# Performance work log

Hardware: AMD Instinct MI355X
Metric: run time of the kernel (lower is better)

## Reference

```python
import jax, jax.numpy as jnp
import numpy as np

B, T, C = 4, 4096, 512


def setup_inputs() -> dict:
    key = jax.random.key(0)
    ks = jax.random.split(key, 7)
    s = 1.0 / np.sqrt(C)  # ~ torch Linear init scale
    X = jax.random.normal(ks[0], (B, T, C), jnp.float32)
    S_n = jnp.zeros((B, C, C), jnp.float32)
    W_Q = jax.random.normal(ks[1], (C, C), jnp.float32) * s
    b_Q = jax.random.normal(ks[2], (C,), jnp.float32) * s
    W_K = jax.random.normal(ks[3], (C, C), jnp.float32) * s
    b_K = jax.random.normal(ks[4], (C,), jnp.float32) * s
    W_V = jax.random.normal(ks[5], (C, C), jnp.float32) * s
    b_V = jax.random.normal(ks[6], (C,), jnp.float32) * s
    return {"X": X, "S_n": S_n, "W_Q": W_Q, "b_Q": b_Q,
            "W_K": W_K, "b_K": b_K, "W_V": W_V, "b_V": b_V}


def reference(X, S_n, W_Q, b_Q, W_K, b_K, W_V, b_V):
    # forward_chunkwise with chunk_len = 1 (exact simplification):
    #   per step t (gamma g_t from linspace(0.96, 0.99, T)):
    #     inner_t = (q_t . k_t) * v_t            # D = gamma^0 = 1
    #     cross_t = (q_t @ S) * g_t              # e[:,0,:] = g^1
    #     O_t     = tanh(inner_t + cross_t)
    #     S      <- k_t^T v_t + g_t * S          # D[-1] = 1, g**chunk_len = g
    Bx, Tx, Cx = X.shape
    Q = X @ W_Q + b_Q  # [B,T,C]
    K = X @ W_K + b_K
    V = X @ W_V + b_V
    gammas = jnp.linspace(0.96, 0.99, Tx).astype(X.dtype)

    def step(S, inp):
        q, k, v, g = inp  # q,k,v: [B,C]; g: scalar
        inner = jnp.sum(q * k, axis=-1, keepdims=True) * v      # [B,C]
        cross = jnp.einsum('bc,bcd->bd', q, S) * g              # [B,C]
        O = jnp.tanh(inner + cross)
        S_new = jnp.einsum('bc,bd->bcd', k, v) + S * g          # [B,C,C]
        return S_new, O

    # original resets S_n to zeros regardless of the passed-in value
    S0 = jnp.zeros_like(S_n)
    S_final, O = jax.lax.scan(
        step, S0,
        (Q.transpose(1, 0, 2), K.transpose(1, 0, 2), V.transpose(1, 0, 2), gammas))
    out = O.transpose(1, 0, 2)  # [B,T,C]
    return out, S_final
```

## Files before the change

### kernel.cpp

```cpp
#include <hip/hip_runtime.h>
#include <math.h>

#define Bsz  4
#define Tlen 4096
#define Cdim 512
#define CUT  (-12.0f)
#define NBE  8388608

typedef unsigned int u32;
typedef _Float16 f16;
typedef __attribute__((ext_vector_type(8))) _Float16 f16x8;
typedef __attribute__((ext_vector_type(4))) float floatx4;
#define MFMA_F16(a,b,c) __builtin_amdgcn_mfma_f32_16x16x32_f16((a),(b),(c),0,0,0)

union pun8 { uint4 u; f16x8 f; };

__device__ __forceinline__ u32 pack2(f16 a, f16 b) {
    return (u32)__builtin_bit_cast(unsigned short, a) |
           ((u32)__builtin_bit_cast(unsigned short, b) << 16);
}
__device__ __forceinline__ u32 splitpack(float v) {
    f16 h = (f16)v;
    f16 l = (f16)(v - (float)h);
    return pack2(h, l);
}
__device__ __forceinline__ void unpack8(const u32* p, f16x8& h, f16x8& l) {
    uint4 q0 = *(const uint4*)p;
    uint4 q1 = *(const uint4*)(p + 4);
    pun8 ph, pl;
    ph.u.x = __builtin_amdgcn_perm(q0.y, q0.x, 0x05040100u);
    pl.u.x = __builtin_amdgcn_perm(q0.y, q0.x, 0x07060302u);
    ph.u.y = __builtin_amdgcn_perm(q0.w, q0.z, 0x05040100u);
    pl.u.y = __builtin_amdgcn_perm(q0.w, q0.z, 0x07060302u);
    ph.u.z = __builtin_amdgcn_perm(q1.y, q1.x, 0x05040100u);
    pl.u.z = __builtin_amdgcn_perm(q1.y, q1.x, 0x07060302u);
    ph.u.w = __builtin_amdgcn_perm(q1.w, q1.z, 0x05040100u);
    pl.u.w = __builtin_amdgcn_perm(q1.w, q1.z, 0x07060302u);
    h = ph.f; l = pl.f;
}
__device__ __forceinline__ float tanh_fast(float x) {
    return 1.0f - 2.0f / (__expf(2.0f * x) + 1.0f);
}

__global__ __launch_bounds__(256) void prep_kernel(
    const float* __restrict__ X,
    const float* __restrict__ WQ, const float* __restrict__ WK,
    const float* __restrict__ WV,
    f16* __restrict__ Xf, f16* __restrict__ WT,
    float* __restrict__ Lg, float* __restrict__ Wfin, int* __restrict__ sLo) {
    __shared__ char pshm[18432];
    int bid = blockIdx.x, tid = threadIdx.x;
    if (bid < 2048) {
        size_t i = ((size_t)bid * 256 + tid) * 16;
        float v[16];
#pragma unroll
        for (int j = 0; j < 4; ++j) {
            float4 a = *(const float4*)(X + i + j * 4);
            v[j*4+0]=a.x; v[j*4+1]=a.y; v[j*4+2]=a.z; v[j*4+3]=a.w;
        }
        uint4 o0, o1;
        o0.x = pack2((f16)v[0], (f16)v[1]);   o0.y = pack2((f16)v[2], (f16)v[3]);
        o0.z = pack2((f16)v[4], (f16)v[5]);   o0.w = pack2((f16)v[6], (f16)v[7]);
        o1.x = pack2((f16)v[8], (f16)v[9]);   o1.y = pack2((f16)v[10], (f16)v[11]);
        o1.z = pack2((f16)v[12], (f16)v[13]); o1.w = pack2((f16)v[14], (f16)v[15]);
        *(uint4*)(Xf + i) = o0;
        *(uint4*)(Xf + i + 8) = o1;
    } else if (bid < 2240) {
        f16* tile = (f16*)pshm;
        int wb = bid - 2048;
        int mat = wb >> 6, rem = wb & 63;
        int k0 = (rem >> 3) * 64, n0 = (rem & 7) * 64;
        const float* W = (mat == 0) ? WQ : (mat == 1) ? WK : WV;
        int row = tid >> 2, q = tid & 3;
        const float* src = W + (size_t)(k0 + row) * Cdim + n0 + q * 16;
        float vv[16];
#pragma unroll
        for (int j = 0; j < 4; ++j) {
            float4 v = *(const float4*)(src + j * 4);
            vv[j*4+0]=v.x; vv[j*4+1]=v.y; vv[j*4+2]=v.z; vv[j*4+3]=v.w;
        }
#pragma unroll
        for (int j = 0; j < 16; ++j) tile[(q * 16 + j) * 72 + row] = (f16)vv[j];
        __syncthreads();
        f16x8 r0 = *(const f16x8*)(tile + row * 72 + q * 16);
        f16x8 r1 = *(const f16x8*)(tile + row * 72 + q * 16 + 8);
        f16* dst = WT + ((size_t)mat * Cdim + n0 + row) * Cdim + k0 + q * 16;
        *(f16x8*)dst = r0;
        *(f16x8*)(dst + 8) = r1;
    } else {
        float* Lsh = (float*)pshm;
        float* sums = (float*)(pshm + 16400);
        float lg[16];
        float local = 0.f;
        int base = tid * 16;
#pragma unroll
        for (int i = 0; i < 16; ++i) {
            int t = base + i;
            float g = 0.96f + 0.03f * ((float)t * (1.0f / 4095.0f));
            lg[i] = logf(g);
            local += lg[i];
        }
        sums[tid] = local;
        __syncthreads();
        for (int off = 1; off < 256; off <<= 1) {
            float v = sums[tid];
            if (tid >= off) v += sums[tid - off];
            __syncthreads();
            sums[tid] = v;
            __syncthreads();
        }
        float pre = (tid == 0) ? 0.f : sums[tid - 1];
#pragma unroll
        for (int i = 0; i < 16; ++i) {
            Lsh[base + i] = pre;
            pre += lg[i];
        }
        if (tid == 255) Lsh[4096] = pre;
        __syncthreads();
        for (int t = tid; t < 4097; t += 256) Lg[t] = Lsh[t];
        float LT = Lsh[4096];
        for (int s = tid; s < 4096; s += 256) Wfin[s] = __expf(LT - Lsh[s + 1]);
        if (tid < 128) {
            float ref = Lsh[tid * 32 + 1];
            int st_hi = tid >> 2;
            int lo = st_hi;
            for (int st = 0; st < st_hi; ++st)
                if (ref - Lsh[st * 128 + 128] > CUT) { lo = st; break; }
            sLo[tid] = lo;
        }
    }
}

__global__ __launch_bounds__(256, 2) void qkv_mfma(
    const f16* __restrict__ Xf, const f16* __restrict__ WT,
    const float* __restrict__ bQ, const float* __restrict__ bK,
    const float* __restrict__ bV,
    f16* __restrict__ Qf, f16* __restrict__ Kf,
    f16* __restrict__ KT, f16* __restrict__ VT) {
    __shared__ char smem[34816];
    u32* sX = (u32*)smem;
    u32* sW = (u32*)(smem + 16384);
    f16* sB = (f16*)smem;
    f16* T  = (f16*)smem;

    int tid = threadIdx.x, lane = tid & 63, wid = tid >> 6;
    int l16 = lane & 15, quad = lane >> 4;
    int wm = wid & 1, wn = wid >> 1;
    int xb = blockIdx.x;
    int mat = xb >> 2, n0 = (xb & 3) * 128;
    int m0 = blockIdx.y * 128;

    floatx4 acc[4][4];
#pragma unroll
    for (int i = 0; i < 4; ++i)
#pragma unroll
        for (int j = 0; j < 4; ++j) acc[i][j] = (floatx4)0.f;

    int srow = tid >> 1, shalf = tid & 1;
    int arow_a = wm * 64 + l16, arow_b = wn * 64 + l16;
    int swz_f = (l16 & 7) << 2;

    for (int kc = 0; kc < Cdim; kc += 64) {
        __syncthreads();
        {
            const f16* gx = Xf + (size_t)(m0 + srow) * Cdim + kc + shalf * 32;
            const f16* gw = WT + ((size_t)(mat * Cdim) + n0 + srow) * Cdim + kc + shalf * 32;
            int wswz = (srow & 7) << 2;
#pragma unroll
            for (int k = 0; k < 4; ++k) {
                uint4 xv = *(const uint4*)(gx + k * 8);
                uint4 wv = *(const uint4*)(gw + k * 8);
                int w = shalf * 16 + k * 4;
                *(uint4*)&sX[srow * 32 + (w ^ wswz)] = xv;
                *(uint4*)&sW[srow * 32 + (w ^ wswz)] = wv;
            }
        }
        __syncthreads();
#pragma unroll
        for (int ks = 0; ks < 2; ++ks) {
            int w0 = ks * 16 + quad * 4;
            f16x8 af[4], bf[4];
#pragma unroll
            for (int mt = 0; mt < 4; ++mt)
                af[mt] = ((pun8*)&sX[(arow_a + mt * 16) * 32 + (w0 ^ swz_f)])->f;
#pragma unroll
            for (int nt = 0; nt < 4; ++nt)
                bf[nt] = ((pun8*)&sW[(arow_b + nt * 16) * 32 + (w0 ^ swz_f)])->f;
#pragma unroll
            for (int mt = 0; mt < 4; ++mt)
#pragma unroll
                for (int nt = 0; nt < 4; ++nt)
                    acc[mt][nt] = MFMA_F16(af[mt], bf[nt], acc[mt][nt]);
        }
    }

    const float* bias = (mat == 0) ? bQ : (mat == 1) ? bK : bV;
    float bv[4];
#pragma unroll
    for (int nt = 0; nt < 4; ++nt) bv[nt] = bias[n0 + wn * 64 + nt * 16 + l16];
    float cv[4][4][4];
#pragma unroll
    for (int mt = 0; mt < 4; ++mt)
#pragma unroll
        for (int nt = 0; nt < 4; ++nt)
#pragma unroll
            for (int r = 0; r < 4; ++r) cv[mt][nt][r] = acc[mt][nt][r] + bv[nt];

    int b = m0 >> 12, tloc = m0 & 4095;

    if (mat == 2) {
        __syncthreads();
#pragma unroll
        for (int mt = 0; mt < 4; ++mt)
#pragma unroll
            for (int nt = 0; nt < 4; ++nt) {
                int dl = wn * 64 + nt * 16 + l16;
                int tl = wm * 64 + mt * 16 + quad * 4;
                *(u32*)(T + dl * 134 + tl)     = pack2((f16)cv[mt][nt][0], (f16)cv[mt][nt][1]);
                *(u32*)(T + dl * 134 + tl + 2) = pack2((f16)cv[mt][nt][2], (f16)cv[mt][nt][3]);
            }
        __syncthreads();
#pragma unroll 8
        for (int dd = 0; dd < 32; ++dd) {
            int dl = wid * 32 + dd;
            u32 v = *(const u32*)(T + dl * 134 + lane * 2);
            *(u32*)(VT + ((size_t)(b * Cdim + n0 + dl)) * Tlen + tloc + lane * 2) = v;
        }
    } else {
        __syncthreads();
#pragma unroll
        for (int mt = 0; mt < 4; ++mt)
#pragma unroll
            for (int nt = 0; nt < 4; ++nt)
#pragma unroll
                for (int r = 0; r < 4; ++r)
                    sB[(wm * 64 + mt * 16 + quad * 4 + r) * 136 +
                       wn * 64 + nt * 16 + l16] = (f16)cv[mt][nt][r];
        __syncthreads();
        {
            f16* Out = (mat == 0) ? Qf : Kf;
            int r2 = tid >> 1, h2 = tid & 1;
            f16* dst = Out + (size_t)(m0 + r2) * Cdim + n0 + h2 * 64;
#pragma unroll
            for (int j = 0; j < 8; ++j)
                *(uint4*)(dst + j * 8) = *(const uint4*)(sB + r2 * 136 + h2 * 64 + j * 8);
        }
        if (mat == 1) {
            __syncthreads();
#pragma unroll
            for (int mt = 0; mt < 4; ++mt)
#pragma unroll
                for (int nt = 0; nt < 4; ++nt) {
                    int dl = wn * 64 + nt * 16 + l16;
                    int tl = wm * 64 + mt * 16 + quad * 4;
                    *(u32*)(T + dl * 134 + tl)     = pack2((f16)cv[mt][nt][0], (f16)cv[mt][nt][1]);
                    *(u32*)(T + dl * 134 + tl + 2) = pack2((f16)cv[mt][nt][2], (f16)cv[mt][nt][3]);
                }
            __syncthreads();
#pragma unroll 8
            for (int dd = 0; dd < 32; ++dd) {
                int dl = wid * 32 + dd;
                u32 v = *(const u32*)(T + dl * 134 + lane * 2);
                *(u32*)(KT + ((size_t)(b * Cdim + n0 + dl)) * Tlen + tloc + lane * 2) = v;
            }
        }
    }
}

__global__ __launch_bounds__(512, 4) void attn_mfma(
    const f16* __restrict__ Qf, const f16* __restrict__ Kf,
    const f16* __restrict__ VT, const float* __restrict__ Lg,
    const int* __restrict__ sLo, float* __restrict__ out) {
    __shared__ char smem[49664];
    u32* sQ  = (u32*)smem;
    u32* sPc = (u32*)(smem + 32768);

    int tid = threadIdx.x, lane = tid & 63, wid = tid >> 6;
    int l16 = lane & 15, quad = lane >> 4;

    int i = blockIdx.x;
    int halfsel = i >> 8, q = i & 255;
    int L = ((q & 7) << 5) | (q >> 3);
    int b = L >> 6, ttl = L & 63;
    int tt = halfsel ? (63 - ttl) : (64 + ttl);
    int t0 = tt * 32;
    size_t bT = (size_t)b * Tlen;
    int lo = sLo[tt], hi = tt >> 2;

    {
        int r = tid >> 4, c16 = tid & 15;
        const f16* src = Qf + (bT + t0 + r) * Cdim + c16 * 32;
        int wswz = (r & 7) << 2;
#pragma unroll
        for (int k = 0; k < 4; ++k) {
            uint4 v = *(const uint4*)(src + k * 8);
            int w = c16 * 16 + k * 4;
            *(uint4*)&sQ[r * 256 + (w ^ wswz)] = v;
        }
    }

    float aT[2][4];
#pragma unroll
    for (int mt = 0; mt < 2; ++mt)
#pragma unroll
        for (int r = 0; r < 4; ++r)
            aT[mt][r] = Lg[t0 + mt * 16 + quad * 4 + r + 1];

    floatx4 oacc[2][4];
#pragma unroll
    for (int mt = 0; mt < 2; ++mt)
#pragma unroll
        for (int nt = 0; nt < 4; ++nt) oacc[mt][nt] = (floatx4)0.f;

    int swz_f = (l16 & 7) << 2;
    int rowA0 = l16 * 256;
    int rowA1 = (16 + l16) * 256;

    __syncthreads();

    for (int st = lo; st <= hi; ++st) {
        int s0 = st * 128;
        float lsp = Lg[s0 + wid * 16 + l16 + 1];

        floatx4 pacc[2];
        pacc[0] = (floatx4)0.f; pacc[1] = (floatx4)0.f;

        const f16* kb = Kf + (bT + s0 + wid * 16 + l16) * Cdim;
#pragma unroll 4
        for (int kc = 0; kc < 16; ++kc) {
            int ko = kc * 32 + quad * 8;
            int w0 = kc * 16 + quad * 4;
            f16x8 a0 = ((pun8*)&sQ[rowA0 + (w0 ^ swz_f)])->f;
            f16x8 a1 = ((pun8*)&sQ[rowA1 + (w0 ^ swz_f)])->f;
            f16x8 bk = *(const f16x8*)(kb + ko);
            pacc[0] = MFMA_F16(a0, bk, pacc[0]);
            pacc[1] = MFMA_F16(a1, bk, pacc[1]);
        }

        __syncthreads();
#pragma unroll
        for (int mt = 0; mt < 2; ++mt)
#pragma unroll
            for (int r = 0; r < 4; ++r) {
                int tl = mt * 16 + quad * 4 + r;
                int sl = wid * 16 + l16;
                int t = t0 + tl, s = s0 + sl;
                float p = pacc[mt][r];
                p = (s <= t) ? p * __expf(aT[mt][r] - lsp) : 0.f;
                sPc[tl * 132 + (sl ^ ((tl & 7) << 4))] = splitpack(p);
            }
        __syncthreads();

        const f16* vb = VT + ((size_t)(b * Cdim + wid * 64 + l16)) * Tlen + s0;
#pragma unroll
        for (int kf = 0; kf < 4; ++kf) {
            int sb = kf * 32 + quad * 8;
            f16x8 ph[2], pl[2];
#pragma unroll
            for (int mt = 0; mt < 2; ++mt) {
                int tl = mt * 16 + l16;
                unpack8(&sPc[tl * 132 + (sb ^ ((tl & 7) << 4))], ph[mt], pl[mt]);
            }
#pragma unroll
            for (int nt = 0; nt < 4; ++nt) {
                f16x8 vf = *(const f16x8*)(vb + (size_t)nt * 16 * Tlen + sb);
#pragma unroll
                for (int mt = 0; mt < 2; ++mt) {
                    oacc[mt][nt] = MFMA_F16(ph[mt], vf, oacc[mt][nt]);
                    oacc[mt][nt] = MFMA_F16(pl[mt], vf, oacc[mt][nt]);
                }
            }
        }
    }

#pragma unroll
    for (int mt = 0; mt < 2; ++mt)
#pragma unroll
        for (int nt = 0; nt < 4; ++nt)
#pragma unroll
            for (int r = 0; r < 4; ++r) {
                int t = t0 + mt * 16 + quad * 4 + r;
                int d = wid * 64 + nt * 16 + l16;
                out[(bT + t) * (size_t)Cdim + d] = tanh_fast(oacc[mt][nt][r]);
            }
}

__global__ __launch_bounds__(256) void sfinal_mfma(
    const f16* __restrict__ KT, const f16* __restrict__ VT,
    const float* __restrict__ Lg, const float* __restrict__ Wfin,
    float* __restrict__ S) {
    __shared__ f16 sA[64 * 72];
    __shared__ f16 sB2[128 * 72];
    int tid = threadIdx.x, lane = tid & 63, wid = tid >> 6;
    int l16 = lane & 15, quad = lane >> 4;
    int wv_c = wid >> 1, wv_d = wid & 1;
    int c0 = blockIdx.x * 64, d0 = blockIdx.y * 128, bb = blockIdx.z;
    float LT = Lg[Tlen];
    floatx4 acc[2][4];
#pragma unroll
    for (int i = 0; i < 2; ++i)
#pragma unroll
        for (int jj = 0; jj < 4; ++jj) acc[i][jj] = (floatx4)0.f;

    int s0start = Tlen - 64;
    for (int s0 = 0; s0 < Tlen; s0 += 64)
        if (LT - Lg[s0 + 64] > CUT) { s0start = s0; break; }

    int rowA = tid >> 2, qA = (tid & 3) * 16;
    int rowB = tid >> 1, qB = (tid & 1) * 32;
    for (int s0 = s0start; s0 < Tlen; s0 += 64) {
        __syncthreads();
        {
            const f16* g = KT + ((size_t)(bb * Cdim + c0 + rowA)) * Tlen + s0 + qA;
            f16x8 u0 = *(const f16x8*)g;
            f16x8 u1 = *(const f16x8*)(g + 8);
            float wv[16];
#pragma unroll
            for (int jj = 0; jj < 4; ++jj) {
                float4 w4 = *(const float4*)(Wfin + s0 + qA + jj * 4);
                wv[jj*4+0]=w4.x; wv[jj*4+1]=w4.y; wv[jj*4+2]=w4.z; wv[jj*4+3]=w4.w;
            }
            f16x8 o0, o1;
#pragma unroll
            for (int jj = 0; jj < 8; ++jj) o0[jj] = (f16)((float)u0[jj] * wv[jj]);
#pragma unroll
            for (int jj = 0; jj < 8; ++jj) o1[jj] = (f16)((float)u1[jj] * wv[8 + jj]);
            *(f16x8*)(sA + rowA * 72 + qA) = o0;
            *(f16x8*)(sA + rowA * 72 + qA + 8) = o1;
            const f16* gv = VT + ((size_t)(bb * Cdim + d0 + rowB)) * Tlen + s0 + qB;
#pragma unroll
            for (int jj = 0; jj < 4; ++jj)
                *(uint4*)(sB2 + rowB * 72 + qB + jj * 8) = *(const uint4*)(gv + jj * 8);
        }
        __syncthreads();
#pragma unroll
        for (int ks = 0; ks < 2; ++ks) {
            int ko = ks * 32 + quad * 8;
            f16x8 av[2], bv2[4];
#pragma unroll
            for (int ct = 0; ct < 2; ++ct)
                av[ct] = *(const f16x8*)(sA + (wv_c * 32 + ct * 16 + l16) * 72 + ko);
#pragma unroll
            for (int dt = 0; dt < 4; ++dt)
                bv2[dt] = *(const f16x8*)(sB2 + (wv_d * 64 + dt * 16 + l16) * 72 + ko);
#pragma unroll
            for (int ct = 0; ct < 2; ++ct)
#pragma unroll
                for (int dt = 0; dt < 4; ++dt)
                    acc[ct][dt] = MFMA_F16(av[ct], bv2[dt], acc[ct][dt]);
        }
    }
#pragma unroll
    for (int ct = 0; ct < 2; ++ct)
#pragma unroll
        for (int dt = 0; dt < 4; ++dt)
#pragma unroll
            for (int r = 0; r < 4; ++r) {
                int c = c0 + wv_c * 32 + ct * 16 + quad * 4 + r;
                int d = d0 + wv_d * 64 + dt * 16 + l16;
                S[((size_t)(bb * Cdim + c)) * Cdim + d] = acc[ct][dt][r];
            }
}

extern "C" void kernel_launch(void* const* d_in, const int* in_sizes, int n_in,
                              void* d_out, int out_size, void* d_ws, size_t ws_size,
                              hipStream_t stream) {
    (void)in_sizes; (void)n_in; (void)out_size; (void)ws_size;
    const float* X  = (const float*)d_in[0];
    const float* WQ = (const float*)d_in[2];
    const float* bQ = (const float*)d_in[3];
    const float* WK = (const float*)d_in[4];
    const float* bK = (const float*)d_in[5];
    const float* WV = (const float*)d_in[6];
    const float* bV = (const float*)d_in[7];

    float* out   = (float*)d_out;
    float* S_out = out + (size_t)NBE;

    char* ws = (char*)d_ws;
    f16*   Xf   = (f16*)(ws);
    f16*   Qf   = (f16*)(ws + 2ull * NBE);
    f16*   Kf   = (f16*)(ws + 4ull * NBE);
    f16*   KT   = (f16*)(ws + 6ull * NBE);
    f16*   VT   = (f16*)(ws + 8ull * NBE);
    f16*   WT   = (f16*)(ws + 10ull * NBE);
    char*  tail = ws + 10ull * NBE + (2u << 20);
    float* Lg   = (float*)(tail);
    float* Wfin = (float*)(tail + 16512);
    int*   sLo  = (int*)(tail + 16512 + 16384);

    prep_kernel<<<2241, 256, 0, stream>>>(X, WQ, WK, WV, Xf, WT, Lg, Wfin, sLo);
    qkv_mfma<<<dim3(12, 128), 256, 0, stream>>>(Xf, WT, bQ, bK, bV, Qf, Kf, KT, VT);
    attn_mfma<<<512, 512, 0, stream>>>(Qf, Kf, VT, Lg, sLo, out);
    sfinal_mfma<<<dim3(8, 4, Bsz), 256, 0, stream>>>(KT, VT, Lg, Wfin, S_out);
}
```

Baseline: 264.8 us.

## Halve attention query tile to 16 rows and double block count

The chunked attention kernel now processes 16 query rows per block instead of 32. It launches 1024 blocks with half the shared memory and a higher occupancy bound, and the per-tile band start indices are recomputed for 256 tiles. The aim is better load balance across CUs for the causal, band-limited workload and more resident waves. In exchange, each K and V fragment loaded from global memory is reused across half as many query rows, which raises total K/V traffic.

```diff
diff --git a/kernel.cpp b/kernel.cpp
--- a/kernel.cpp
+++ b/kernel.cpp
@@ -120,9 +120,9 @@
         for (int t = tid; t < 4097; t += 256) Lg[t] = Lsh[t];
         float LT = Lsh[4096];
         for (int s = tid; s < 4096; s += 256) Wfin[s] = __expf(LT - Lsh[s + 1]);
-        if (tid < 128) {
-            float ref = Lsh[tid * 32 + 1];
-            int st_hi = tid >> 2;
+        {
+            float ref = Lsh[tid * 16 + 1];
+            int st_hi = tid >> 3;
             int lo = st_hi;
             for (int st = 0; st < st_hi; ++st)
                 if (ref - Lsh[st * 128 + 128] > CUT) { lo = st; break; }
@@ -267,54 +267,49 @@
     }
 }
 
-__global__ __launch_bounds__(512, 4) void attn_mfma(
+__global__ __launch_bounds__(512, 8) void attn_mfma(
     const f16* __restrict__ Qf, const f16* __restrict__ Kf,
     const f16* __restrict__ VT, const float* __restrict__ Lg,
     const int* __restrict__ sLo, float* __restrict__ out) {
-    __shared__ char smem[49664];
-    u32* sQ  = (u32*)smem;
-    u32* sPc = (u32*)(smem + 32768);
+    __shared__ char smem[24832];
+    u32* sQ = (u32*)smem;
+    u32* sP = (u32*)(smem + 16384);
 
     int tid = threadIdx.x, lane = tid & 63, wid = tid >> 6;
     int l16 = lane & 15, quad = lane >> 4;
 
     int i = blockIdx.x;
-    int halfsel = i >> 8, q = i & 255;
-    int L = ((q & 7) << 5) | (q >> 3);
-    int b = L >> 6, ttl = L & 63;
-    int tt = halfsel ? (63 - ttl) : (64 + ttl);
-    int t0 = tt * 32;
+    int halfsel = i >> 9, q = i & 511;
+    int L = ((q & 7) << 6) | (q >> 3);
+    int b = L >> 7, ttl = L & 127;
+    int tt = halfsel ? (127 - ttl) : (128 + ttl);
+    int t0 = tt * 16;
     size_t bT = (size_t)b * Tlen;
-    int lo = sLo[tt], hi = tt >> 2;
+    int lo = sLo[tt], hi = tt >> 3;
 
     {
-        int r = tid >> 4, c16 = tid & 15;
-        const f16* src = Qf + (bT + t0 + r) * Cdim + c16 * 32;
+        int r = tid >> 5, c = tid & 31;
+        const f16* src = Qf + (bT + t0 + r) * Cdim + c * 16;
         int wswz = (r & 7) << 2;
 #pragma unroll
-        for (int k = 0; k < 4; ++k) {
+        for (int k = 0; k < 2; ++k) {
             uint4 v = *(const uint4*)(src + k * 8);
-            int w = c16 * 16 + k * 4;
+            int w = c * 8 + k * 4;
             *(uint4*)&sQ[r * 256 + (w ^ wswz)] = v;
         }
     }
 
-    float aT[2][4];
-#pragma unroll
-    for (int mt = 0; mt < 2; ++mt)
-#pragma unroll
-        for (int r = 0; r < 4; ++r)
-            aT[mt][r] = Lg[t0 + mt * 16 + quad * 4 + r + 1];
-
-    floatx4 oacc[2][4];
-#pragma unroll
-    for (int mt = 0; mt < 2; ++mt)
-#pragma unroll
-        for (int nt = 0; nt < 4; ++nt) oacc[mt][nt] = (floatx4)0.f;
+    float aT[4];
+#pragma unroll
+    for (int r = 0; r < 4; ++r)
+        aT[r] = Lg[t0 + quad * 4 + r + 1];
+
+    floatx4 oacc[4];
+#pragma unroll
+    for (int nt = 0; nt < 4; ++nt) oacc[nt] = (floatx4)0.f;
 
     int swz_f = (l16 & 7) << 2;
     int rowA0 = l16 * 256;
-    int rowA1 = (16 + l16) * 256;
 
     __syncthreads();
 
@@ -322,8 +317,7 @@
         int s0 = st * 128;
         float lsp = Lg[s0 + wid * 16 + l16 + 1];
 
-        floatx4 pacc[2];
-        pacc[0] = (floatx4)0.f; pacc[1] = (floatx4)0.f;
+        floatx4 pacc = (floatx4)0.f;
 
         const f16* kb = Kf + (bT + s0 + wid * 16 + l16) * Cdim;
 #pragma unroll 4
@@ -331,58 +325,45 @@
             int ko = kc * 32 + quad * 8;
             int w0 = kc * 16 + quad * 4;
             f16x8 a0 = ((pun8*)&sQ[rowA0 + (w0 ^ swz_f)])->f;
-            f16x8 a1 = ((pun8*)&sQ[rowA1 + (w0 ^ swz_f)])->f;
             f16x8 bk = *(const f16x8*)(kb + ko);
-            pacc[0] = MFMA_F16(a0, bk, pacc[0]);
-            pacc[1] = MFMA_F16(a1, bk, pacc[1]);
-        }
-
-        __syncthreads();
-#pragma unroll
-        for (int mt = 0; mt < 2; ++mt)
-#pragma unroll
-            for (int r = 0; r < 4; ++r) {
-                int tl = mt * 16 + quad * 4 + r;
-                int sl = wid * 16 + l16;
-                int t = t0 + tl, s = s0 + sl;
-                float p = pacc[mt][r];
-                p = (s <= t) ? p * __expf(aT[mt][r] - lsp) : 0.f;
-                sPc[tl * 132 + (sl ^ ((tl & 7) << 4))] = splitpack(p);
-            }
+            pacc = MFMA_F16(a0, bk, pacc);
+        }
+
+        __syncthreads();
+#pragma unroll
+        for (int r = 0; r < 4; ++r) {
+            int tl = quad * 4 + r;
+            int sl = wid * 16 + l16;
+            int t = t0 + tl, s = s0 + sl;
+            float p = pacc[r];
+            p = (s <= t) ? p * __expf(aT[r] - lsp) : 0.f;
+            sP[tl * 132 + (sl ^ ((tl & 7) << 4))] = splitpack(p);
+        }
         __syncthreads();
 
         const f16* vb = VT + ((size_t)(b * Cdim + wid * 64 + l16)) * Tlen + s0;
 #pragma unroll
         for (int kf = 0; kf < 4; ++kf) {
             int sb = kf * 32 + quad * 8;
-            f16x8 ph[2], pl[2];
-#pragma unroll
-            for (int mt = 0; mt < 2; ++mt) {
-                int tl = mt * 16 + l16;
-                unpack8(&sPc[tl * 132 + (sb ^ ((tl & 7) << 4))], ph[mt], pl[mt]);
-            }
+            f16x8 ph, pl;
+            unpack8(&sP[l16 * 132 + (sb ^ ((l16 & 7) << 4))], ph, pl);
 #pragma unroll
             for (int nt = 0; nt < 4; ++nt) {
                 f16x8 vf = *(const f16x8*)(vb + (size_t)nt * 16 * Tlen + sb);
-#pragma unroll
-                for (int mt = 0; mt < 2; ++mt) {
-                    oacc[mt][nt] = MFMA_F16(ph[mt], vf, oacc[mt][nt]);
-                    oacc[mt][nt] = MFMA_F16(pl[mt], vf, oacc[mt][nt]);
-                }
-            }
-        }
-    }
-
-#pragma unroll
-    for (int mt = 0; mt < 2; ++mt)
-#pragma unroll
-        for (int nt = 0; nt < 4; ++nt)
-#pragma unroll
-            for (int r = 0; r < 4; ++r) {
-                int t = t0 + mt * 16 + quad * 4 + r;
-                int d = wid * 64 + nt * 16 + l16;
-                out[(bT + t) * (size_t)Cdim + d] = tanh_fast(oacc[mt][nt][r]);
-            }
+                oacc[nt] = MFMA_F16(ph, vf, oacc[nt]);
+                oacc[nt] = MFMA_F16(pl, vf, oacc[nt]);
+            }
+        }
+    }
+
+#pragma unroll
+    for (int nt = 0; nt < 4; ++nt)
+#pragma unroll
+        for (int r = 0; r < 4; ++r) {
+            int t = t0 + quad * 4 + r;
+            int d = wid * 64 + nt * 16 + l16;
+            out[(bT + t) * (size_t)Cdim + d] = tanh_fast(oacc[nt][r]);
+        }
 }
 
 __global__ __launch_bounds__(256) void sfinal_mfma(
@@ -491,6 +472,6 @@
 
     prep_kernel<<<2241, 256, 0, stream>>>(X, WQ, WK, WV, Xf, WT, Lg, Wfin, sLo);
     qkv_mfma<<<dim3(12, 128), 256, 0, stream>>>(Xf, WT, bQ, bK, bV, Qf, Kf, KT, VT);
-    attn_mfma<<<512, 512, 0, stream>>>(Qf, Kf, VT, Lg, sLo, out);
+    attn_mfma<<<1024, 512, 0, stream>>>(Qf, Kf, VT, Lg, sLo, out);
     sfinal_mfma<<<dim3(8, 4, Bsz), 256, 0, stream>>>(KT, VT, Lg, Wfin, S_out);
 }
```

New measurement: 333.5 us. 26.0% more time.
